# Optimization experiments

Measured on AMD Instinct MI355X. Metric: run time of the kernel, lower is better.

## Reference

```python
import jax, jax.numpy as jnp
import numpy as np


def setup_inputs() -> dict:
    key = jax.random.key(0)
    k1, k2, k3, k4 = jax.random.split(key, 4)
    B, S, DIN, DOUT = 4, 2048, 4096, 4096
    x = jax.random.normal(k1, (B, S, DIN), dtype=jnp.float32)
    # base is already transposed in the module: [in_features, out_features]
    base = jax.random.normal(k2, (DIN, DOUT), dtype=jnp.float32) * 0.02
    # logical 0/1 bit mask (unpacked view of the packed binary mask), [in, out]
    mask = jax.random.randint(k3, (DIN, DOUT), 0, 2, dtype=jnp.int32)
    # learned scalar coefficient (mean |diff| quantile at init)
    coeff = jax.random.uniform(k4, (), dtype=jnp.float32) * 0.01
    return {"x": x, "base": base, "mask": mask, "coeff": coeff}


def reference(x, base, mask, coeff):
    # binary_bmm: bit 1 -> +1, bit 0 -> -1 sign matrix, shared across batch
    sign = (2 * mask - 1).astype(x.dtype)          # [in, out]
    dense = jnp.einsum("bsi,io->bso", x, base)     # standard dense matmul
    binary = jnp.einsum("bsi,io->bso", x, sign)    # 1-bit (sign) matmul
    return dense + coeff * binary
```

## Files before the change

### kernel.cpp

```cpp
#include <hip/hip_runtime.h>
#include <hip/hip_bf16.h>
#include <stdint.h>


typedef short bf16x8_t __attribute__((ext_vector_type(8)));
typedef float f32x4_t __attribute__((ext_vector_type(4)));
typedef unsigned short u16x8_t __attribute__((ext_vector_type(8)));

#define GLD_LDS16(gptr, lptr)                                                        \
  __builtin_amdgcn_global_load_lds(                                                  \
      (const __attribute__((address_space(1))) void*)(gptr),                         \
      (__attribute__((address_space(3))) void*)(lptr), 16, 0, 0)

#define MFMA_BF16 __builtin_amdgcn_mfma_f32_16x16x32_bf16

__global__ __launch_bounds__(256) void cast_x_kernel(const float* __restrict__ x,
                                                     __hip_bfloat16* __restrict__ xb) {
  size_t i = ((size_t)blockIdx.x * 256 + threadIdx.x) * 8;
  f32x4_t v0 = *(const f32x4_t*)&x[i];
  f32x4_t v1 = *(const f32x4_t*)&x[i + 4];
  __hip_bfloat16 tmp[8];
#pragma unroll
  for (int j = 0; j < 4; ++j) tmp[j] = __float2bfloat16(v0[j]);
#pragma unroll
  for (int j = 0; j < 4; ++j) tmp[4 + j] = __float2bfloat16(v1[j]);
  *(u16x8_t*)&xb[i] = *(const u16x8_t*)tmp;
}

__global__ __launch_bounds__(256) void make_wt_kernel(const float* __restrict__ base,
                                                      const int* __restrict__ mask,
                                                      const float* __restrict__ coeffp,
                                                      __hip_bfloat16* __restrict__ wt,
                                                      int K, int N) {
  __shared__ float tile[32][33];
  const float coeff = coeffp[0];
  const int n0 = blockIdx.x * 32, k0 = blockIdx.y * 32;
  const int tx = threadIdx.x & 31;
  const int ty = threadIdx.x >> 5;
#pragma unroll
  for (int j = 0; j < 4; ++j) {
    int k = k0 + ty + j * 8;
    size_t idx = (size_t)k * N + n0 + tx;
    float b = base[idx];
    int m = mask[idx];
    tile[ty + j * 8][tx] = b + (m ? coeff : -coeff);
  }
  __syncthreads();
#pragma unroll
  for (int j = 0; j < 4; ++j) {
    int n = n0 + ty + j * 8;
    wt[(size_t)n * K + k0 + tx] = __float2bfloat16(tile[tx][ty + j * 8]);
  }
}

__global__ __launch_bounds__(512, 2) void gemm256_kernel(const __hip_bfloat16* __restrict__ xb,
                                                         const __hip_bfloat16* __restrict__ wt,
                                                         float* __restrict__ out,
                                                         int M, int N, int K) {
  __shared__ __align__(16) __hip_bfloat16 As[2 * 256 * 64];
  __shared__ __align__(16) __hip_bfloat16 Bs[2 * 256 * 64];
  const int NT = K >> 6;

  const int nwg = gridDim.x;
  int bid = blockIdx.x;
  int sw = bid;
  if ((nwg & 7) == 0) {
    int per = nwg >> 3;
    sw = (bid & 7) * per + (bid >> 3);
  }
  const int ntn = N >> 8;
  const int tm = sw / ntn, tn = sw - tm * ntn;
  const int m0 = tm << 8, n0 = tn << 8;

  const int tid = threadIdx.x;
  const int lane = tid & 63;
  const int wave = tid >> 6;
  const int wr = wave >> 2;
  const int wc = wave & 3;

  const int lrow = lane >> 3;
  const int lcol = ((lane & 7) ^ lrow) << 3;
  uint32_t aOff[2][2], bOff[2][2];
#pragma unroll
  for (int h = 0; h < 2; ++h)
#pragma unroll
    for (int j = 0; j < 2; ++j) {
      aOff[h][j] = (uint32_t)((m0 + h * 128 + wave * 16 + j * 8 + lrow) * K + lcol);
      bOff[h][j] = (uint32_t)((n0 + h * 128 + wave * 16 + j * 8 + lrow) * K + lcol);
    }

#define STAGE_A(h, j, tau)                                                       \
  GLD_LDS16(xb + (size_t)aOff[h][j] + (size_t)(tau) * 64,                        \
            (char*)As + (((tau) & 1) << 15) + ((h) * 16384 + wave * 2048 + (j) * 1024))
#define STAGE_B(h, j, tau)                                                       \
  GLD_LDS16(wt + (size_t)bOff[h][j] + (size_t)(tau) * 64,                        \
            (char*)Bs + (((tau) & 1) << 15) + ((h) * 16384 + wave * 2048 + (j) * 1024))

  STAGE_A(0, 0, 0); STAGE_A(0, 1, 0);
  STAGE_A(1, 0, 0); STAGE_A(1, 1, 0);
  STAGE_B(0, 0, 0); STAGE_B(0, 1, 0);
  STAGE_B(1, 0, 0); STAGE_B(1, 1, 0);
  STAGE_A(0, 0, 1); STAGE_A(0, 1, 1);
  asm volatile("s_waitcnt vmcnt(2)" ::: "memory");
  __builtin_amdgcn_s_barrier();

  const int lane15 = lane & 15;
  const int swz = (lane & 7) << 4;
  const int c0 = (((lane >> 4) << 4)) ^ swz;
  const int c1 = (64 + ((lane >> 4) << 4)) ^ swz;
  const int aRowB = (wr * 128 + lane15) * 128;
  const int bRowB = (wc * 64 + lane15) * 128;

  f32x4_t acc[8][4];
  const f32x4_t zero = {0.0f, 0.0f, 0.0f, 0.0f};
#pragma unroll
  for (int i = 0; i < 8; ++i)
#pragma unroll
    for (int j = 0; j < 4; ++j) acc[i][j] = zero;

  bf16x8_t aL[4][2], aH[4][2], bL[2][2], bH[2][2];

  for (int t = 0; t < NT; ++t) {
    const int p = t & 1;
    const char* a0 = (const char*)As + (p << 15) + aRowB;
    const char* b0 = (const char*)Bs + (p << 15) + bRowB;

#pragma unroll
    for (int mi = 0; mi < 4; ++mi) {
      aL[mi][0] = *(const bf16x8_t*)(a0 + mi * 2048 + c0);
      aL[mi][1] = *(const bf16x8_t*)(a0 + mi * 2048 + c1);
    }
#pragma unroll
    for (int ni = 0; ni < 2; ++ni) {
      bL[ni][0] = *(const bf16x8_t*)(b0 + ni * 2048 + c0);
      bL[ni][1] = *(const bf16x8_t*)(b0 + ni * 2048 + c1);
    }
    if (t + 1 < NT) { STAGE_A(1, 0, t + 1); STAGE_A(1, 1, t + 1); }
    __builtin_amdgcn_s_barrier();
    asm volatile("s_waitcnt lgkmcnt(0)" ::: "memory");
    __builtin_amdgcn_sched_barrier(0);
    __builtin_amdgcn_s_setprio(1);
#pragma unroll
    for (int mi = 0; mi < 4; ++mi)
#pragma unroll
      for (int ni = 0; ni < 2; ++ni) {
        acc[mi][ni] = MFMA_BF16(aL[mi][0], bL[ni][0], acc[mi][ni], 0, 0, 0);
        acc[mi][ni] = MFMA_BF16(aL[mi][1], bL[ni][1], acc[mi][ni], 0, 0, 0);
      }
    __builtin_amdgcn_s_setprio(0);
    __builtin_amdgcn_s_barrier();

#pragma unroll
    for (int ni = 0; ni < 2; ++ni) {
      bH[ni][0] = *(const bf16x8_t*)(b0 + (ni + 2) * 2048 + c0);
      bH[ni][1] = *(const bf16x8_t*)(b0 + (ni + 2) * 2048 + c1);
    }
    if (t + 1 < NT) { STAGE_B(0, 0, t + 1); STAGE_B(0, 1, t + 1); }
    __builtin_amdgcn_s_barrier();
    asm volatile("s_waitcnt lgkmcnt(0)" ::: "memory");
    __builtin_amdgcn_sched_barrier(0);
    __builtin_amdgcn_s_setprio(1);
#pragma unroll
    for (int mi = 0; mi < 4; ++mi)
#pragma unroll
      for (int ni = 0; ni < 2; ++ni) {
        acc[mi][ni + 2] = MFMA_BF16(aL[mi][0], bH[ni][0], acc[mi][ni + 2], 0, 0, 0);
        acc[mi][ni + 2] = MFMA_BF16(aL[mi][1], bH[ni][1], acc[mi][ni + 2], 0, 0, 0);
      }
    __builtin_amdgcn_s_setprio(0);
    __builtin_amdgcn_s_barrier();

#pragma unroll
    for (int mi = 0; mi < 4; ++mi) {
      aH[mi][0] = *(const bf16x8_t*)(a0 + (mi + 4) * 2048 + c0);
      aH[mi][1] = *(const bf16x8_t*)(a0 + (mi + 4) * 2048 + c1);
    }
    if (t + 1 < NT) { STAGE_B(1, 0, t + 1); STAGE_B(1, 1, t + 1); }
    __builtin_amdgcn_s_barrier();
    asm volatile("s_waitcnt lgkmcnt(0)" ::: "memory");
    __builtin_amdgcn_sched_barrier(0);
    __builtin_amdgcn_s_setprio(1);
#pragma unroll
    for (int mi = 0; mi < 4; ++mi)
#pragma unroll
      for (int ni = 0; ni < 2; ++ni) {
        acc[mi + 4][ni + 2] = MFMA_BF16(aH[mi][0], bH[ni][0], acc[mi + 4][ni + 2], 0, 0, 0);
        acc[mi + 4][ni + 2] = MFMA_BF16(aH[mi][1], bH[ni][1], acc[mi + 4][ni + 2], 0, 0, 0);
      }
    __builtin_amdgcn_s_setprio(0);
    __builtin_amdgcn_s_barrier();

    if (t + 2 < NT) {
      STAGE_A(0, 0, t + 2); STAGE_A(0, 1, t + 2);
      asm volatile("s_waitcnt vmcnt(2)" ::: "memory");
    } else {
      asm volatile("s_waitcnt vmcnt(0)" ::: "memory");
    }
    __builtin_amdgcn_s_barrier();
    __builtin_amdgcn_sched_barrier(0);
    __builtin_amdgcn_s_setprio(1);
#pragma unroll
    for (int mi = 0; mi < 4; ++mi)
#pragma unroll
      for (int ni = 0; ni < 2; ++ni) {
        acc[mi + 4][ni] = MFMA_BF16(aH[mi][0], bL[ni][0], acc[mi + 4][ni], 0, 0, 0);
        acc[mi + 4][ni] = MFMA_BF16(aH[mi][1], bL[ni][1], acc[mi + 4][ni], 0, 0, 0);
      }
    __builtin_amdgcn_s_setprio(0);
    __builtin_amdgcn_s_barrier();
  }

  const int row0 = m0 + wr * 128 + (lane >> 4) * 4;
  const int col0 = n0 + wc * 64 + lane15;
#pragma unroll
  for (int mi = 0; mi < 8; ++mi)
#pragma unroll
    for (int ni = 0; ni < 4; ++ni) {
#pragma unroll
      for (int k = 0; k < 4; ++k)
        out[(size_t)(row0 + mi * 16 + k) * N + col0 + ni * 16] = acc[mi][ni][k];
    }
#undef STAGE_A
#undef STAGE_B
}

__global__ __launch_bounds__(256) void gemm_fallback_kernel(const float* __restrict__ x,
                                                            const float* __restrict__ base,
                                                            const int* __restrict__ mask,
                                                            const float* __restrict__ coeffp,
                                                            float* __restrict__ out,
                                                            int M, int N, int K) {
  __shared__ __align__(16) __hip_bfloat16 As[128 * 32];
  __shared__ __align__(16) __hip_bfloat16 Bs[128 * 32];
  const float coeff = coeffp[0];
  const int ntn = N >> 7;
  const int tm = blockIdx.x / ntn, tn = blockIdx.x - tm * ntn;
  const int m0 = tm << 7, n0 = tn << 7;
  const int tid = threadIdx.x, lane = tid & 63, wave = tid >> 6;
  const int wr = wave >> 1, wc = wave & 1;

  f32x4_t acc[4][4];
  const f32x4_t zero = {0.0f, 0.0f, 0.0f, 0.0f};
#pragma unroll
  for (int i = 0; i < 4; ++i)
#pragma unroll
    for (int j = 0; j < 4; ++j) acc[i][j] = zero;

  const int arow = tid >> 1;
  const int acol = (tid & 1) * 16;
  const int bkk = tid & 31;
  const int bnb = (tid >> 5) * 16;
  const int arow_base = wr * 64 + (lane & 15);
  const int bcol_base = wc * 64 + (lane & 15);
  const int koff = (lane >> 4) * 8;

  for (int k0 = 0; k0 < K; k0 += 32) {
    __syncthreads();
    {
      const float* src = &x[(size_t)(m0 + arow) * K + k0 + acol];
      __hip_bfloat16 tmp[16];
#pragma unroll
      for (int j = 0; j < 16; ++j) tmp[j] = __float2bfloat16(src[j]);
      *(u16x8_t*)&As[arow * 32 + acol] = *(const u16x8_t*)&tmp[0];
      *(u16x8_t*)&As[arow * 32 + acol + 8] = *(const u16x8_t*)&tmp[8];
    }
    {
      const float* bsrc = &base[(size_t)(k0 + bkk) * N + n0 + bnb];
      const int* msrc = &mask[(size_t)(k0 + bkk) * N + n0 + bnb];
#pragma unroll
      for (int j = 0; j < 16; ++j) {
        float w = bsrc[j] + (msrc[j] ? coeff : -coeff);
        Bs[(bnb + j) * 32 + bkk] = __float2bfloat16(w);
      }
    }
    __syncthreads();

    bf16x8_t a[4], b[4];
#pragma unroll
    for (int mi = 0; mi < 4; ++mi)
      a[mi] = *(const bf16x8_t*)&As[(arow_base + mi * 16) * 32 + koff];
#pragma unroll
    for (int ni = 0; ni < 4; ++ni)
      b[ni] = *(const bf16x8_t*)&Bs[(bcol_base + ni * 16) * 32 + koff];
#pragma unroll
    for (int mi = 0; mi < 4; ++mi)
#pragma unroll
      for (int ni = 0; ni < 4; ++ni)
        acc[mi][ni] = MFMA_BF16(a[mi], b[ni], acc[mi][ni], 0, 0, 0);
  }

  const int row0 = m0 + wr * 64 + (lane >> 4) * 4;
  const int col0 = n0 + wc * 64 + (lane & 15);
#pragma unroll
  for (int mi = 0; mi < 4; ++mi)
#pragma unroll
    for (int ni = 0; ni < 4; ++ni) {
      int r = row0 + mi * 16;
      int c = col0 + ni * 16;
#pragma unroll
      for (int k = 0; k < 4; ++k) out[(size_t)(r + k) * N + c] = acc[mi][ni][k];
    }
}

extern "C" void kernel_launch(void* const* d_in, const int* in_sizes, int n_in,
                              void* d_out, int out_size, void* d_ws, size_t ws_size,
                              hipStream_t stream) {
  const int B = 4, S = 2048, DIN = 4096, DOUT = 4096;
  const int M = B * S;
  const float* x = (const float*)d_in[0];
  const float* base = (const float*)d_in[1];
  const int* mask = (const int*)d_in[2];
  const float* coeff = (const float*)d_in[3];
  float* out = (float*)d_out;

  const size_t xb_bytes = (size_t)M * DIN * sizeof(__hip_bfloat16);
  const size_t wt_bytes = (size_t)DIN * DOUT * sizeof(__hip_bfloat16);

  if (ws_size >= xb_bytes + wt_bytes) {
    __hip_bfloat16* xb = (__hip_bfloat16*)d_ws;
    __hip_bfloat16* wt = (__hip_bfloat16*)((char*)d_ws + xb_bytes);
    cast_x_kernel<<<(M * DIN) / (256 * 8), 256, 0, stream>>>(x, xb);
    make_wt_kernel<<<dim3(DOUT / 32, DIN / 32), 256, 0, stream>>>(base, mask, coeff, wt, DIN, DOUT);
    const int n_tiles = (M / 256) * (DOUT / 256);
    gemm256_kernel<<<n_tiles, 512, 0, stream>>>(xb, wt, out, M, DOUT, DIN);
  } else {
    const int n_tiles = (M / 128) * (DOUT / 128);
    gemm_fallback_kernel<<<n_tiles, 256, 0, stream>>>(x, base, mask, coeff, out, M, DOUT, DIN);
  }
}
```

Before: 343.6 us.

## Switch main GEMM from 16x16x32 to 32x32x16 bf16 MFMA tiles

Replaces the 16x16x32 MFMA instruction grid with 32x32x16 bf16 MFMAs, regrouping LDS fragment loads into four k-slices per 32-row group and remapping the accumulator layout and output store indexing. Larger MFMA tiles mean fewer LDS fragment reads per flop and fewer instructions issued per k-step. The LDS swizzle now has to serve the new 32-lane access pattern, which may introduce bank conflicts. The output store also writes rows in a strided pattern. The final-iteration wait is narrowed to skip a redundant vmcnt(0) once no loads remain.

```diff
diff --git a/kernel.cpp b/kernel.cpp
--- a/kernel.cpp
+++ b/kernel.cpp
@@ -5,6 +5,7 @@
 
 typedef short bf16x8_t __attribute__((ext_vector_type(8)));
 typedef float f32x4_t __attribute__((ext_vector_type(4)));
+typedef float f32x16_t __attribute__((ext_vector_type(16)));
 typedef unsigned short u16x8_t __attribute__((ext_vector_type(8)));
 
 #define GLD_LDS16(gptr, lptr)                                                        \
@@ -12,6 +13,7 @@
       (const __attribute__((address_space(1))) void*)(gptr),                         \
       (__attribute__((address_space(3))) void*)(lptr), 16, 0, 0)
 
+#define MFMA32 __builtin_amdgcn_mfma_f32_32x32x16_bf16
 #define MFMA_BF16 __builtin_amdgcn_mfma_f32_16x16x32_bf16
 
 __global__ __launch_bounds__(256) void cast_x_kernel(const float* __restrict__ x,
@@ -104,21 +106,24 @@
   asm volatile("s_waitcnt vmcnt(2)" ::: "memory");
   __builtin_amdgcn_s_barrier();
 
-  const int lane15 = lane & 15;
+  const int lane31 = lane & 31;
   const int swz = (lane & 7) << 4;
-  const int c0 = (((lane >> 4) << 4)) ^ swz;
-  const int c1 = (64 + ((lane >> 4) << 4)) ^ swz;
-  const int aRowB = (wr * 128 + lane15) * 128;
-  const int bRowB = (wc * 64 + lane15) * 128;
-
-  f32x4_t acc[8][4];
-  const f32x4_t zero = {0.0f, 0.0f, 0.0f, 0.0f};
-#pragma unroll
-  for (int i = 0; i < 8; ++i)
-#pragma unroll
-    for (int j = 0; j < 4; ++j) acc[i][j] = zero;
-
-  bf16x8_t aL[4][2], aH[4][2], bL[2][2], bH[2][2];
+  const int kb = (lane >> 5) << 4;
+  int cb[4];
+#pragma unroll
+  for (int s = 0; s < 4; ++s) cb[s] = (s * 32 + kb) ^ swz;
+  const int aRowB = (wr * 128 + lane31) * 128;
+  const int bRowB = (wc * 64 + lane31) * 128;
+
+  f32x16_t acc[4][2];
+#pragma unroll
+  for (int i = 0; i < 4; ++i)
+#pragma unroll
+    for (int j = 0; j < 2; ++j)
+#pragma unroll
+      for (int e = 0; e < 16; ++e) acc[i][j][e] = 0.0f;
+
+  bf16x8_t aL[2][4], aH[2][4], bL[4], bH[4];
 
   for (int t = 0; t < NT; ++t) {
     const int p = t & 1;
@@ -126,99 +131,87 @@
     const char* b0 = (const char*)Bs + (p << 15) + bRowB;
 
 #pragma unroll
-    for (int mi = 0; mi < 4; ++mi) {
-      aL[mi][0] = *(const bf16x8_t*)(a0 + mi * 2048 + c0);
-      aL[mi][1] = *(const bf16x8_t*)(a0 + mi * 2048 + c1);
-    }
-#pragma unroll
-    for (int ni = 0; ni < 2; ++ni) {
-      bL[ni][0] = *(const bf16x8_t*)(b0 + ni * 2048 + c0);
-      bL[ni][1] = *(const bf16x8_t*)(b0 + ni * 2048 + c1);
-    }
+    for (int g = 0; g < 2; ++g)
+#pragma unroll
+      for (int s = 0; s < 4; ++s)
+        aL[g][s] = *(const bf16x8_t*)(a0 + g * 4096 + cb[s]);
+#pragma unroll
+    for (int s = 0; s < 4; ++s) bL[s] = *(const bf16x8_t*)(b0 + cb[s]);
     if (t + 1 < NT) { STAGE_A(1, 0, t + 1); STAGE_A(1, 1, t + 1); }
     __builtin_amdgcn_s_barrier();
     asm volatile("s_waitcnt lgkmcnt(0)" ::: "memory");
     __builtin_amdgcn_sched_barrier(0);
     __builtin_amdgcn_s_setprio(1);
 #pragma unroll
-    for (int mi = 0; mi < 4; ++mi)
-#pragma unroll
-      for (int ni = 0; ni < 2; ++ni) {
-        acc[mi][ni] = MFMA_BF16(aL[mi][0], bL[ni][0], acc[mi][ni], 0, 0, 0);
-        acc[mi][ni] = MFMA_BF16(aL[mi][1], bL[ni][1], acc[mi][ni], 0, 0, 0);
-      }
+    for (int s = 0; s < 4; ++s)
+#pragma unroll
+      for (int g = 0; g < 2; ++g)
+        acc[g][0] = MFMA32(aL[g][s], bL[s], acc[g][0], 0, 0, 0);
     __builtin_amdgcn_s_setprio(0);
     __builtin_amdgcn_s_barrier();
 
 #pragma unroll
-    for (int ni = 0; ni < 2; ++ni) {
-      bH[ni][0] = *(const bf16x8_t*)(b0 + (ni + 2) * 2048 + c0);
-      bH[ni][1] = *(const bf16x8_t*)(b0 + (ni + 2) * 2048 + c1);
-    }
+    for (int s = 0; s < 4; ++s) bH[s] = *(const bf16x8_t*)(b0 + 4096 + cb[s]);
     if (t + 1 < NT) { STAGE_B(0, 0, t + 1); STAGE_B(0, 1, t + 1); }
     __builtin_amdgcn_s_barrier();
     asm volatile("s_waitcnt lgkmcnt(0)" ::: "memory");
     __builtin_amdgcn_sched_barrier(0);
     __builtin_amdgcn_s_setprio(1);
 #pragma unroll
-    for (int mi = 0; mi < 4; ++mi)
-#pragma unroll
-      for (int ni = 0; ni < 2; ++ni) {
-        acc[mi][ni + 2] = MFMA_BF16(aL[mi][0], bH[ni][0], acc[mi][ni + 2], 0, 0, 0);
-        acc[mi][ni + 2] = MFMA_BF16(aL[mi][1], bH[ni][1], acc[mi][ni + 2], 0, 0, 0);
-      }
+    for (int s = 0; s < 4; ++s)
+#pragma unroll
+      for (int g = 0; g < 2; ++g)
+        acc[g][1] = MFMA32(aL[g][s], bH[s], acc[g][1], 0, 0, 0);
     __builtin_amdgcn_s_setprio(0);
     __builtin_amdgcn_s_barrier();
 
 #pragma unroll
-    for (int mi = 0; mi < 4; ++mi) {
-      aH[mi][0] = *(const bf16x8_t*)(a0 + (mi + 4) * 2048 + c0);
-      aH[mi][1] = *(const bf16x8_t*)(a0 + (mi + 4) * 2048 + c1);
-    }
+    for (int g = 0; g < 2; ++g)
+#pragma unroll
+      for (int s = 0; s < 4; ++s)
+        aH[g][s] = *(const bf16x8_t*)(a0 + (g + 2) * 4096 + cb[s]);
     if (t + 1 < NT) { STAGE_B(1, 0, t + 1); STAGE_B(1, 1, t + 1); }
     __builtin_amdgcn_s_barrier();
     asm volatile("s_waitcnt lgkmcnt(0)" ::: "memory");
     __builtin_amdgcn_sched_barrier(0);
     __builtin_amdgcn_s_setprio(1);
 #pragma unroll
-    for (int mi = 0; mi < 4; ++mi)
-#pragma unroll
-      for (int ni = 0; ni < 2; ++ni) {
-        acc[mi + 4][ni + 2] = MFMA_BF16(aH[mi][0], bH[ni][0], acc[mi + 4][ni + 2], 0, 0, 0);
-        acc[mi + 4][ni + 2] = MFMA_BF16(aH[mi][1], bH[ni][1], acc[mi + 4][ni + 2], 0, 0, 0);
-      }
+    for (int s = 0; s < 4; ++s)
+#pragma unroll
+      for (int g = 0; g < 2; ++g)
+        acc[g + 2][1] = MFMA32(aH[g][s], bH[s], acc[g + 2][1], 0, 0, 0);
     __builtin_amdgcn_s_setprio(0);
     __builtin_amdgcn_s_barrier();
 
     if (t + 2 < NT) {
       STAGE_A(0, 0, t + 2); STAGE_A(0, 1, t + 2);
       asm volatile("s_waitcnt vmcnt(2)" ::: "memory");
-    } else {
+    } else if (t + 1 < NT) {
       asm volatile("s_waitcnt vmcnt(0)" ::: "memory");
     }
     __builtin_amdgcn_s_barrier();
     __builtin_amdgcn_sched_barrier(0);
     __builtin_amdgcn_s_setprio(1);
 #pragma unroll
-    for (int mi = 0; mi < 4; ++mi)
-#pragma unroll
-      for (int ni = 0; ni < 2; ++ni) {
-        acc[mi + 4][ni] = MFMA_BF16(aH[mi][0], bL[ni][0], acc[mi + 4][ni], 0, 0, 0);
-        acc[mi + 4][ni] = MFMA_BF16(aH[mi][1], bL[ni][1], acc[mi + 4][ni], 0, 0, 0);
+    for (int s = 0; s < 4; ++s)
+#pragma unroll
+      for (int g = 0; g < 2; ++g)
+        acc[g + 2][0] = MFMA32(aH[g][s], bL[s], acc[g + 2][0], 0, 0, 0);
+    __builtin_amdgcn_s_setprio(0);
+    __builtin_amdgcn_s_barrier();
+  }
+
+  const int row0 = m0 + wr * 128 + 4 * (lane >> 5);
+  const int col0 = n0 + wc * 64 + lane31;
+#pragma unroll
+  for (int mi = 0; mi < 4; ++mi)
+#pragma unroll
+    for (int ni = 0; ni < 2; ++ni) {
+#pragma unroll
+      for (int reg = 0; reg < 16; ++reg) {
+        int r = row0 + mi * 32 + (reg & 3) + 8 * (reg >> 2);
+        out[(size_t)r * N + col0 + ni * 32] = acc[mi][ni][reg];
       }
-    __builtin_amdgcn_s_setprio(0);
-    __builtin_amdgcn_s_barrier();
-  }
-
-  const int row0 = m0 + wr * 128 + (lane >> 4) * 4;
-  const int col0 = n0 + wc * 64 + lane15;
-#pragma unroll
-  for (int mi = 0; mi < 8; ++mi)
-#pragma unroll
-    for (int ni = 0; ni < 4; ++ni) {
-#pragma unroll
-      for (int k = 0; k < 4; ++k)
-        out[(size_t)(row0 + mi * 16 + k) * N + col0 + ni * 16] = acc[mi][ni][k];
     }
 #undef STAGE_A
 #undef STAGE_B
```

Measured after the change: 362.7 us. +5.6%, slower.

## Merge four MFMA phases per K-tile into two with fewer barriers

Applied to the files above, without the earlier changes.

The GEMM main loop is restructured from four compute phases per K-iteration, each wrapped by barriers and LDS waits, into two phases. All B fragments (low and high) are now read up front, and all next-tile staging of A-high and both B halves is issued in the first phase. The goal is to cut barrier and wait overhead and give the MFMA issue longer uninterrupted runs. The cost is higher register pressure from holding bH alongside the other fragments, and coarser interleaving of global-to-LDS traffic with compute. The final-iteration vmcnt handling also changes.

```diff
diff --git a/kernel.cpp b/kernel.cpp
--- a/kernel.cpp
+++ b/kernel.cpp
@@ -134,8 +134,14 @@
     for (int ni = 0; ni < 2; ++ni) {
       bL[ni][0] = *(const bf16x8_t*)(b0 + ni * 2048 + c0);
       bL[ni][1] = *(const bf16x8_t*)(b0 + ni * 2048 + c1);
-    }
-    if (t + 1 < NT) { STAGE_A(1, 0, t + 1); STAGE_A(1, 1, t + 1); }
+      bH[ni][0] = *(const bf16x8_t*)(b0 + (ni + 2) * 2048 + c0);
+      bH[ni][1] = *(const bf16x8_t*)(b0 + (ni + 2) * 2048 + c1);
+    }
+    if (t + 1 < NT) {
+      STAGE_A(1, 0, t + 1); STAGE_A(1, 1, t + 1);
+      STAGE_B(0, 0, t + 1); STAGE_B(0, 1, t + 1);
+      STAGE_B(1, 0, t + 1); STAGE_B(1, 1, t + 1);
+    }
     __builtin_amdgcn_s_barrier();
     asm volatile("s_waitcnt lgkmcnt(0)" ::: "memory");
     __builtin_amdgcn_sched_barrier(0);
@@ -146,24 +152,6 @@
       for (int ni = 0; ni < 2; ++ni) {
         acc[mi][ni] = MFMA_BF16(aL[mi][0], bL[ni][0], acc[mi][ni], 0, 0, 0);
         acc[mi][ni] = MFMA_BF16(aL[mi][1], bL[ni][1], acc[mi][ni], 0, 0, 0);
-      }
-    __builtin_amdgcn_s_setprio(0);
-    __builtin_amdgcn_s_barrier();
-
-#pragma unroll
-    for (int ni = 0; ni < 2; ++ni) {
-      bH[ni][0] = *(const bf16x8_t*)(b0 + (ni + 2) * 2048 + c0);
-      bH[ni][1] = *(const bf16x8_t*)(b0 + (ni + 2) * 2048 + c1);
-    }
-    if (t + 1 < NT) { STAGE_B(0, 0, t + 1); STAGE_B(0, 1, t + 1); }
-    __builtin_amdgcn_s_barrier();
-    asm volatile("s_waitcnt lgkmcnt(0)" ::: "memory");
-    __builtin_amdgcn_sched_barrier(0);
-    __builtin_amdgcn_s_setprio(1);
-#pragma unroll
-    for (int mi = 0; mi < 4; ++mi)
-#pragma unroll
-      for (int ni = 0; ni < 2; ++ni) {
         acc[mi][ni + 2] = MFMA_BF16(aL[mi][0], bH[ni][0], acc[mi][ni + 2], 0, 0, 0);
         acc[mi][ni + 2] = MFMA_BF16(aL[mi][1], bH[ni][1], acc[mi][ni + 2], 0, 0, 0);
       }
@@ -175,7 +163,12 @@
       aH[mi][0] = *(const bf16x8_t*)(a0 + (mi + 4) * 2048 + c0);
       aH[mi][1] = *(const bf16x8_t*)(a0 + (mi + 4) * 2048 + c1);
     }
-    if (t + 1 < NT) { STAGE_B(1, 0, t + 1); STAGE_B(1, 1, t + 1); }
+    if (t + 2 < NT) {
+      STAGE_A(0, 0, t + 2); STAGE_A(0, 1, t + 2);
+      asm volatile("s_waitcnt vmcnt(2)" ::: "memory");
+    } else if (t + 1 < NT) {
+      asm volatile("s_waitcnt vmcnt(0)" ::: "memory");
+    }
     __builtin_amdgcn_s_barrier();
     asm volatile("s_waitcnt lgkmcnt(0)" ::: "memory");
     __builtin_amdgcn_sched_barrier(0);
@@ -186,23 +179,6 @@
       for (int ni = 0; ni < 2; ++ni) {
         acc[mi + 4][ni + 2] = MFMA_BF16(aH[mi][0], bH[ni][0], acc[mi + 4][ni + 2], 0, 0, 0);
         acc[mi + 4][ni + 2] = MFMA_BF16(aH[mi][1], bH[ni][1], acc[mi + 4][ni + 2], 0, 0, 0);
-      }
-    __builtin_amdgcn_s_setprio(0);
-    __builtin_amdgcn_s_barrier();
-
-    if (t + 2 < NT) {
-      STAGE_A(0, 0, t + 2); STAGE_A(0, 1, t + 2);
-      asm volatile("s_waitcnt vmcnt(2)" ::: "memory");
-    } else {
-      asm volatile("s_waitcnt vmcnt(0)" ::: "memory");
-    }
-    __builtin_amdgcn_s_barrier();
-    __builtin_amdgcn_sched_barrier(0);
-    __builtin_amdgcn_s_setprio(1);
-#pragma unroll
-    for (int mi = 0; mi < 4; ++mi)
-#pragma unroll
-      for (int ni = 0; ni < 2; ++ni) {
         acc[mi + 4][ni] = MFMA_BF16(aH[mi][0], bL[ni][0], acc[mi + 4][ni], 0, 0, 0);
         acc[mi + 4][ni] = MFMA_BF16(aH[mi][1], bL[ni][1], acc[mi + 4][ni], 0, 0, 0);
       }
```

Result: faster. 316.1 us (-8.0%).
